# Performance work log

Measured on AMD Instinct MI355X. Metric: run time of the kernel, lower is better.

Reference implementation:

```python
import jax, jax.numpy as jnp
import numpy as np
from jax import lax


def _ramp_filter_real(size):
    # torch ramp_filter: spatial-domain ramp, FFT is purely real (even symmetric)
    image_n = np.concatenate([np.arange(1, size // 2 + 1, 2),
                              np.arange(size // 2 - 1, 0, -2)]).astype(np.float64)
    f = np.zeros(size, dtype=np.float64)
    f[0] = 0.25
    f[1::2] = -1.0 / (np.pi * image_n) ** 2
    return (2.0 * np.real(np.fft.fft(f))).astype(np.float32)  # [size]


def setup_inputs() -> dict:
    key = jax.random.key(0)
    # sinogram: [B, C, detector_bins, n_angles]
    x = jax.random.normal(key, (4, 1, 512, 180), dtype=jnp.float32)
    return {"x": x}


def reference(x):
    B, C, S, A = x.shape  # S = in_size = it_size (circle=True), A = n_angles
    # ---- ramp filtering along detector axis (axis=2) ----
    pad_to = max(64, 1 << int(np.ceil(np.log2(2 * S))))
    xp = jnp.pad(x, ((0, 0), (0, 0), (0, pad_to - S), (0, 0)))
    ramp = jnp.asarray(_ramp_filter_real(pad_to))
    # original multiplies by complex filter r*(1+i); imag part of ifft is 0 for real x,
    # so real part equals standard ramp filtering
    Xf = jnp.fft.fft(xp, axis=2)
    filt = (ramp * (1.0 + 1.0j)).astype(jnp.complex64)
    xfilt = jnp.real(jnp.fft.ifft(Xf * filt[None, None, :, None], axis=2))
    xfilt = xfilt[:, :, :S, :].astype(x.dtype)  # [B,C,S,A]

    # ---- backprojection ----
    unit = jnp.linspace(-1.0, 1.0, S, dtype=x.dtype)
    ygrid, xgrid = jnp.meshgrid(unit, unit, indexing="ij")  # torch.meshgrid 'ij'
    thetas = (jnp.arange(A, dtype=x.dtype) * (np.pi / 180.0)).astype(x.dtype)
    # t coordinate in [-sqrt2, sqrt2]: [A,S,S]
    t = (xgrid[None] * jnp.cos(thetas)[:, None, None]
         - ygrid[None] * jnp.sin(thetas)[:, None, None])
    # grid_sample bilinear, align_corners=True, zeros padding; X coord selects angle i exactly
    p = (t + 1.0) * 0.5 * (S - 1)
    p0 = jnp.floor(p)
    w = (p - p0).astype(x.dtype)
    i0 = p0.astype(jnp.int32)
    i1 = i0 + 1
    v0 = ((i0 >= 0) & (i0 < S)).astype(x.dtype)
    v1 = ((i1 >= 0) & (i1 < S)).astype(x.dtype)
    i0c = jnp.clip(i0, 0, S - 1)
    i1c = jnp.clip(i1, 0, S - 1)

    xa = jnp.moveaxis(xfilt, 3, 0)  # [A,B,C,S]

    def body(acc, inp):
        xa_a, i0a, i1a, wa, v0a, v1a = inp
        g = (xa_a[:, :, i0a] * v0a * (1.0 - wa)
             + xa_a[:, :, i1a] * v1a * wa)  # [B,C,S,S]
        return acc + g, None

    reco0 = jnp.zeros((B, C, S, S), dtype=x.dtype)
    reco, _ = lax.scan(body, reco0, (xa, i0c, i1c, w, v0, v1))

    # circle mask + normalization
    mask = (xgrid ** 2 + ygrid ** 2) <= 1.0
    reco = jnp.where(mask[None, None], reco, 0.0)
    reco = reco * (np.pi / (2.0 * A))
    return reco
```

## Files before the change

### kernel.cpp

```cpp
#include <hip/hip_runtime.h>
#include <math.h>

namespace {

constexpr int BB  = 4;
constexpr int SS  = 512;
constexpr int AA  = 180;
constexpr int PAD = 112;
constexpr int ROWBUF = SS + 2 * PAD;

__global__ __launch_bounds__(256) void ramp_filter_kernel(
    const float* __restrict__ x, float* __restrict__ xf) {
  __shared__ __align__(16) float xs[2][2][256];
  __shared__ __align__(16) float G[2][528];
  const int t  = threadIdx.x;
  const int a0 = blockIdx.x * 2;
  const int b  = blockIdx.y;

  const float s  = (float)(M_PI / 360.0);
  const float cc = (float)(-2.0 / (M_PI * M_PI)) * s;
  for (int i = t; i < 528; i += 256) {
    { int kk = i;     float d = (float)(2 * kk - 511); G[0][i] = (kk < 512) ? cc / (d * d) : 0.0f; }
    { int kk = i + 1; float d = (float)(2 * kk - 511); G[1][i] = (kk < 512) ? cc / (d * d) : 0.0f; }
  }

  const float* xb = x + (size_t)b * (SS * AA) + a0;
  {
    int m = t;
    float2 v = *(const float2*)(xb + (size_t)m * AA);
    xs[0][m & 1][m >> 1] = v.x;  xs[1][m & 1][m >> 1] = v.y;
    m = t + 256;
    float2 v2 = *(const float2*)(xb + (size_t)m * AA);
    xs[0][m & 1][m >> 1] = v2.x; xs[1][m & 1][m >> 1] = v2.y;
  }
  __syncthreads();

  const int col = t >> 7;
  const int p   = (t >> 6) & 1;
  const int idx = t & 63;
  const float* Gp = G[p];
  const float* xv = xs[col][1 - p];

  float acc[4] = {0.f, 0.f, 0.f, 0.f};
  float W[8];
  {
    const int A0 = 4 * idx + 252;
    float4 w0 = *(const float4*)(Gp + A0);
    float4 w1 = *(const float4*)(Gp + A0 + 4);
    W[0] = w0.x; W[1] = w0.y; W[2] = w0.z; W[3] = w0.w;
    W[4] = w1.x; W[5] = w1.y; W[6] = w1.z; W[7] = w1.w;
  }

#pragma unroll
  for (int q = 0; q < 64; ++q) {
    const float4 xq = *(const float4*)(xv + 4 * q);
    float4 nw;
    if (q != 63) nw = *(const float4*)(Gp + (4 * idx + 252 - 4 * (q + 1)));
#pragma unroll
    for (int r = 0; r < 4; ++r) {
      acc[r] = fmaf(W[3 + r], xq.x, acc[r]);
      acc[r] = fmaf(W[2 + r], xq.y, acc[r]);
      acc[r] = fmaf(W[1 + r], xq.z, acc[r]);
      acc[r] = fmaf(W[0 + r], xq.w, acc[r]);
    }
    if (q != 63) {
      W[7] = W[3]; W[6] = W[2]; W[5] = W[1]; W[4] = W[0];
      W[0] = nw.x; W[1] = nw.y; W[2] = nw.z; W[3] = nw.w;
    }
  }

  const float selfc = 0.5f * s;
  const float* xsp = xs[col][p];
  float* orow = xf + ((size_t)(b * AA + a0 + col)) * SS;
#pragma unroll
  for (int r = 0; r < 4; ++r) {
    orow[p + 8 * idx + 2 * r] = fmaf(selfc, xsp[4 * idx + r], acc[r]);
  }
}

__global__ __launch_bounds__(256) void backproject_kernel(
    const float* __restrict__ xf, float* __restrict__ out) {
  __shared__ __align__(16) float rows[2][3][ROWBUF];
  __shared__ float2 trig_s[45];

  const int t     = threadIdx.x;
  const int w     = t >> 6;
  const int lane  = t & 63;
  const int tx    = blockIdx.x;
  const int ty    = blockIdx.y;
  const int b     = blockIdx.z >> 2;
  const int chunk = blockIdx.z & 3;
  const int a0    = chunk * 45;

  for (int i = t; i < 2 * 3 * 2 * PAD; i += 256) {
    int rr = i / (2 * PAD);
    int o  = i - rr * (2 * PAD);
    int off = (o < PAD) ? o : (o + SS);
    rows[rr / 3][rr % 3][off] = 0.0f;
  }
  if (t < 45) {
    float th = (float)(a0 + t) * (float)(M_PI / 180.0);
    float sn, cn;
    sincosf(th, &sn, &cn);
    trig_s[t] = make_float2(cn * 255.5f, sn * 255.5f);
  }

  const float* xf_src = xf + ((size_t)b * AA + a0) * SS;

  auto stage = [&](int g, int buf) {
    const float* base = xf_src + (size_t)(g * 3) * SS;
    {
      const int s = w;
      const float* gp = base + (s >> 1) * SS + (s & 1) * 256 + lane * 4;
      void* lp = (void*)&rows[buf][s >> 1][PAD + (s & 1) * 256];
      __builtin_amdgcn_global_load_lds(
          (const __attribute__((address_space(1))) void*)gp,
          (__attribute__((address_space(3))) void*)lp, 16, 0, 0);
    }
    if (w < 2) {
      const int s = 4 + w;
      const float* gp = base + (s >> 1) * SS + (s & 1) * 256 + lane * 4;
      void* lp = (void*)&rows[buf][s >> 1][PAD + (s & 1) * 256];
      __builtin_amdgcn_global_load_lds(
          (const __attribute__((address_space(1))) void*)gp,
          (__attribute__((address_space(3))) void*)lp, 16, 0, 0);
    }
  };

  const int gx = tx * 64 + lane;
  const float step = 2.0f / 511.0f;
  const float xg = __fadd_rn(-1.0f, __fmul_rn((float)gx, step));
  float dy[8];
#pragma unroll
  for (int kk = 0; kk < 8; ++kk) {
    int gy = ty * 32 + w + 4 * kk;
    dy[kk] = -__fadd_rn(-1.0f, __fmul_rn((float)gy, step));
  }

  const float Kp = 255.5f + (float)PAD;
  float acc[8] = {0.f, 0.f, 0.f, 0.f, 0.f, 0.f, 0.f, 0.f};

  stage(0, 0);
  __syncthreads();

  int buf = 0;
  for (int g = 0; g < 15; ++g) {
    if (g + 1 < 15) stage(g + 1, buf ^ 1);
#pragma unroll
    for (int aa = 0; aa < 3; ++aa) {
      const float2 cs = trig_s[g * 3 + aa];
      const float base = fmaf(xg, cs.x, Kp);
      const float* R = rows[buf][aa];
#pragma unroll
      for (int kk = 0; kk < 8; ++kk) {
        float p  = fmaf(dy[kk], cs.y, base);
        int   i0 = (int)p;
#if __has_builtin(__builtin_amdgcn_fractf)
        float wt = __builtin_amdgcn_fractf(p);
#else
        float wt = p - floorf(p);
#endif
        float v0 = R[i0];
        float v1 = R[i0 + 1];
        acc[kk] = fmaf(wt, v1 - v0, acc[kk] + v0);
      }
    }
    __syncthreads();
    buf ^= 1;
  }

  const float xx = __fmul_rn(xg, xg);
#pragma unroll
  for (int kk = 0; kk < 8; ++kk) {
    float ss = __fadd_rn(xx, __fmul_rn(dy[kk], dy[kk]));
    if (ss <= 1.0f) {
      int gy = ty * 32 + w + 4 * kk;
      unsafeAtomicAdd(&out[((size_t)b * SS + gy) * SS + gx], acc[kk]);
    }
  }
}

}

extern "C" void kernel_launch(void* const* d_in, const int* in_sizes, int n_in,
                              void* d_out, int out_size, void* d_ws, size_t ws_size,
                              hipStream_t stream) {
  const float* x   = (const float*)d_in[0];
  float*       out = (float*)d_out;
  float*       xf  = (float*)d_ws;

  hipMemsetAsync(d_out, 0, (size_t)out_size * sizeof(float), stream);
  ramp_filter_kernel<<<dim3(AA / 2, BB), 256, 0, stream>>>(x, xf);
  backproject_kernel<<<dim3(8, 16, 16), 256, 0, stream>>>(xf, out);
}
```

Before: 106.9 us.

## Fuse zeroing, ramp filter and backprojection into one cooperative kernel

Replaces the memset plus two kernel launches with a single cooperative-grid kernel of 512 blocks. Each block zeroes part of the output, the first 360 blocks run the ramp filter, and after a grid-wide sync every block runs the backprojection. The backprojection is re-tiled so each thread covers two output columns and 90 angles instead of 45, which halves the number of atomic-add passes. Neighbouring taps are read as one paired LDS load. A two-kernel fallback runs if the cooperative launch fails. The grid sync adds its own cost, and fewer, larger blocks may reduce occupancy.

Result: slower. 218.5 us (+104.5%).

```diff
diff --git a/kernel.cpp b/kernel.cpp
--- a/kernel.cpp
+++ b/kernel.cpp
@@ -1,5 +1,8 @@
 #include <hip/hip_runtime.h>
+#include <hip/hip_cooperative_groups.h>
 #include <math.h>
+
+namespace cg = cooperative_groups;
 
 namespace {
 
@@ -9,37 +12,57 @@
 constexpr int PAD = 112;
 constexpr int ROWBUF = SS + 2 * PAD;
 
-__global__ __launch_bounds__(256) void ramp_filter_kernel(
-    const float* __restrict__ x, float* __restrict__ xf) {
-  __shared__ __align__(16) float xs[2][2][256];
-  __shared__ __align__(16) float G[2][528];
-  const int t  = threadIdx.x;
-  const int a0 = blockIdx.x * 2;
-  const int b  = blockIdx.y;
+struct RampShared {
+  float xs[2][2][256];
+  float G[2][528];
+};
+struct BpShared {
+  float  rows[2][3][ROWBUF];
+  float2 trig[90];
+};
+constexpr size_t SMEM_BYTES =
+    sizeof(BpShared) > sizeof(RampShared) ? sizeof(BpShared) : sizeof(RampShared);
+
+__device__ __forceinline__ float2 lds_load_pair(const float* p) {
+  float2 v;
+  __builtin_memcpy(&v, p, sizeof(float2));
+  return v;
+}
+
+__device__ __forceinline__ void phase0_zero(int bid, int t, float* out) {
+  float4 z = make_float4(0.f, 0.f, 0.f, 0.f);
+  ((float4*)out)[bid * 512 + t]       = z;
+  ((float4*)out)[bid * 512 + 256 + t] = z;
+}
+
+__device__ __forceinline__ void phase1_ramp(int bid, int t, const float* x,
+                                            float* xf, RampShared& S) {
+  const int b  = bid / 90;
+  const int a0 = (bid - b * 90) * 2;
 
   const float s  = (float)(M_PI / 360.0);
   const float cc = (float)(-2.0 / (M_PI * M_PI)) * s;
   for (int i = t; i < 528; i += 256) {
-    { int kk = i;     float d = (float)(2 * kk - 511); G[0][i] = (kk < 512) ? cc / (d * d) : 0.0f; }
-    { int kk = i + 1; float d = (float)(2 * kk - 511); G[1][i] = (kk < 512) ? cc / (d * d) : 0.0f; }
+    { int kk = i;     float d = (float)(2 * kk - 511); S.G[0][i] = (kk < 512) ? cc / (d * d) : 0.0f; }
+    { int kk = i + 1; float d = (float)(2 * kk - 511); S.G[1][i] = (kk < 512) ? cc / (d * d) : 0.0f; }
   }
 
   const float* xb = x + (size_t)b * (SS * AA) + a0;
   {
     int m = t;
     float2 v = *(const float2*)(xb + (size_t)m * AA);
-    xs[0][m & 1][m >> 1] = v.x;  xs[1][m & 1][m >> 1] = v.y;
+    S.xs[0][m & 1][m >> 1] = v.x;  S.xs[1][m & 1][m >> 1] = v.y;
     m = t + 256;
     float2 v2 = *(const float2*)(xb + (size_t)m * AA);
-    xs[0][m & 1][m >> 1] = v2.x; xs[1][m & 1][m >> 1] = v2.y;
+    S.xs[0][m & 1][m >> 1] = v2.x; S.xs[1][m & 1][m >> 1] = v2.y;
   }
   __syncthreads();
 
   const int col = t >> 7;
   const int p   = (t >> 6) & 1;
   const int idx = t & 63;
-  const float* Gp = G[p];
-  const float* xv = xs[col][1 - p];
+  const float* Gp = S.G[p];
+  const float* xv = S.xs[col][1 - p];
 
   float acc[4] = {0.f, 0.f, 0.f, 0.f};
   float W[8];
@@ -70,39 +93,34 @@
   }
 
   const float selfc = 0.5f * s;
-  const float* xsp = xs[col][p];
+  const float* xsp = S.xs[col][p];
   float* orow = xf + ((size_t)(b * AA + a0 + col)) * SS;
 #pragma unroll
-  for (int r = 0; r < 4; ++r) {
+  for (int r = 0; r < 4; ++r)
     orow[p + 8 * idx + 2 * r] = fmaf(selfc, xsp[4 * idx + r], acc[r]);
-  }
-}
-
-__global__ __launch_bounds__(256) void backproject_kernel(
-    const float* __restrict__ xf, float* __restrict__ out) {
-  __shared__ __align__(16) float rows[2][3][ROWBUF];
-  __shared__ float2 trig_s[45];
-
-  const int t     = threadIdx.x;
-  const int w     = t >> 6;
-  const int lane  = t & 63;
-  const int tx    = blockIdx.x;
-  const int ty    = blockIdx.y;
-  const int b     = blockIdx.z >> 2;
-  const int chunk = blockIdx.z & 3;
-  const int a0    = chunk * 45;
+}
+
+__device__ __forceinline__ void phase2_bp(int bid, int t, const float* xf,
+                                          float* out, BpShared& S) {
+  const int tx   = bid & 3;
+  const int ty   = (bid >> 2) & 15;
+  const int z    = bid >> 6;
+  const int b    = z >> 1;
+  const int a0   = (z & 1) * 90;
+  const int w    = t >> 6;
+  const int lane = t & 63;
 
   for (int i = t; i < 2 * 3 * 2 * PAD; i += 256) {
     int rr = i / (2 * PAD);
     int o  = i - rr * (2 * PAD);
     int off = (o < PAD) ? o : (o + SS);
-    rows[rr / 3][rr % 3][off] = 0.0f;
-  }
-  if (t < 45) {
+    S.rows[rr / 3][rr % 3][off] = 0.0f;
+  }
+  if (t < 90) {
     float th = (float)(a0 + t) * (float)(M_PI / 180.0);
     float sn, cn;
     sincosf(th, &sn, &cn);
-    trig_s[t] = make_float2(cn * 255.5f, sn * 255.5f);
+    S.trig[t] = make_float2(cn * 255.5f, sn * 255.5f);
   }
 
   const float* xf_src = xf + ((size_t)b * AA + a0) * SS;
@@ -110,26 +128,27 @@
   auto stage = [&](int g, int buf) {
     const float* base = xf_src + (size_t)(g * 3) * SS;
     {
-      const int s = w;
-      const float* gp = base + (s >> 1) * SS + (s & 1) * 256 + lane * 4;
-      void* lp = (void*)&rows[buf][s >> 1][PAD + (s & 1) * 256];
+      const int sg = w;
+      const float* gp = base + (sg >> 1) * SS + (sg & 1) * 256 + lane * 4;
+      void* lp = (void*)&S.rows[buf][sg >> 1][PAD + (sg & 1) * 256];
       __builtin_amdgcn_global_load_lds(
           (const __attribute__((address_space(1))) void*)gp,
           (__attribute__((address_space(3))) void*)lp, 16, 0, 0);
     }
     if (w < 2) {
-      const int s = 4 + w;
-      const float* gp = base + (s >> 1) * SS + (s & 1) * 256 + lane * 4;
-      void* lp = (void*)&rows[buf][s >> 1][PAD + (s & 1) * 256];
+      const int sg = 4 + w;
+      const float* gp = base + (sg >> 1) * SS + (sg & 1) * 256 + lane * 4;
+      void* lp = (void*)&S.rows[buf][sg >> 1][PAD + (sg & 1) * 256];
       __builtin_amdgcn_global_load_lds(
           (const __attribute__((address_space(1))) void*)gp,
           (__attribute__((address_space(3))) void*)lp, 16, 0, 0);
     }
   };
 
-  const int gx = tx * 64 + lane;
+  const int gx0 = tx * 128 + lane;
   const float step = 2.0f / 511.0f;
-  const float xg = __fadd_rn(-1.0f, __fmul_rn((float)gx, step));
+  const float xg0 = __fadd_rn(-1.0f, __fmul_rn((float)gx0, step));
+  const float xg1 = __fadd_rn(-1.0f, __fmul_rn((float)(gx0 + 64), step));
   float dy[8];
 #pragma unroll
   for (int kk = 0; kk < 8; ++kk) {
@@ -138,46 +157,81 @@
   }
 
   const float Kp = 255.5f + (float)PAD;
-  float acc[8] = {0.f, 0.f, 0.f, 0.f, 0.f, 0.f, 0.f, 0.f};
+  float acc0[8], acc1[8];
+#pragma unroll
+  for (int kk = 0; kk < 8; ++kk) { acc0[kk] = 0.f; acc1[kk] = 0.f; }
 
   stage(0, 0);
   __syncthreads();
 
   int buf = 0;
-  for (int g = 0; g < 15; ++g) {
-    if (g + 1 < 15) stage(g + 1, buf ^ 1);
+  for (int g = 0; g < 30; ++g) {
+    if (g + 1 < 30) stage(g + 1, buf ^ 1);
 #pragma unroll
     for (int aa = 0; aa < 3; ++aa) {
-      const float2 cs = trig_s[g * 3 + aa];
-      const float base = fmaf(xg, cs.x, Kp);
-      const float* R = rows[buf][aa];
+      const float2 cs = S.trig[g * 3 + aa];
+      const float base0 = fmaf(xg0, cs.x, Kp);
+      const float base1 = fmaf(xg1, cs.x, Kp);
+      const float* R = S.rows[buf][aa];
 #pragma unroll
       for (int kk = 0; kk < 8; ++kk) {
-        float p  = fmaf(dy[kk], cs.y, base);
-        int   i0 = (int)p;
+        float p0 = fmaf(dy[kk], cs.y, base0);
+        float p1 = fmaf(dy[kk], cs.y, base1);
+        int   i0 = (int)p0;
+        int   i1 = (int)p1;
 #if __has_builtin(__builtin_amdgcn_fractf)
-        float wt = __builtin_amdgcn_fractf(p);
+        float w0 = __builtin_amdgcn_fractf(p0);
+        float w1 = __builtin_amdgcn_fractf(p1);
 #else
-        float wt = p - floorf(p);
+        float w0 = p0 - floorf(p0);
+        float w1 = p1 - floorf(p1);
 #endif
-        float v0 = R[i0];
-        float v1 = R[i0 + 1];
-        acc[kk] = fmaf(wt, v1 - v0, acc[kk] + v0);
+        float2 ab0 = lds_load_pair(R + i0);
+        float2 ab1 = lds_load_pair(R + i1);
+        acc0[kk] = fmaf(w0, ab0.y - ab0.x, acc0[kk] + ab0.x);
+        acc1[kk] = fmaf(w1, ab1.y - ab1.x, acc1[kk] + ab1.x);
       }
     }
     __syncthreads();
     buf ^= 1;
   }
 
-  const float xx = __fmul_rn(xg, xg);
+  const float xx0 = __fmul_rn(xg0, xg0);
+  const float xx1 = __fmul_rn(xg1, xg1);
 #pragma unroll
   for (int kk = 0; kk < 8; ++kk) {
-    float ss = __fadd_rn(xx, __fmul_rn(dy[kk], dy[kk]));
-    if (ss <= 1.0f) {
-      int gy = ty * 32 + w + 4 * kk;
-      unsafeAtomicAdd(&out[((size_t)b * SS + gy) * SS + gx], acc[kk]);
-    }
-  }
+    int gy = ty * 32 + w + 4 * kk;
+    float yy = __fmul_rn(dy[kk], dy[kk]);
+    float s0 = __fadd_rn(xx0, yy);
+    float s1 = __fadd_rn(xx1, yy);
+    float* orow = out + ((size_t)b * SS + gy) * SS;
+    if (s0 <= 1.0f) unsafeAtomicAdd(&orow[gx0], acc0[kk]);
+    if (s1 <= 1.0f) unsafeAtomicAdd(&orow[gx0 + 64], acc1[kk]);
+  }
+}
+
+__global__ __launch_bounds__(256, 4) void fused_coop(
+    const float* __restrict__ x, float* __restrict__ xf, float* __restrict__ out) {
+  __shared__ __align__(16) char smem[SMEM_BYTES];
+  const int t   = threadIdx.x;
+  const int bid = blockIdx.x;
+  phase0_zero(bid, t, out);
+  if (bid < 360) phase1_ramp(bid, t, x, xf, *(RampShared*)smem);
+  cg::this_grid().sync();
+  phase2_bp(bid, t, xf, out, *(BpShared*)smem);
+}
+
+__global__ __launch_bounds__(256, 4) void k_pre(
+    const float* __restrict__ x, float* __restrict__ xf, float* __restrict__ out) {
+  __shared__ __align__(16) char smem[sizeof(RampShared)];
+  const int t = threadIdx.x, bid = blockIdx.x;
+  phase0_zero(bid, t, out);
+  if (bid < 360) phase1_ramp(bid, t, x, xf, *(RampShared*)smem);
+}
+__global__ __launch_bounds__(256, 4) void k_bp(
+    const float* __restrict__ xf, float* __restrict__ out) {
+  __shared__ __align__(16) char smem[sizeof(BpShared)];
+  phase2_bp(blockIdx.x, threadIdx.x, xf, out, *(BpShared*)smem);
 }
 
 }
@@ -189,7 +243,11 @@
   float*       out = (float*)d_out;
   float*       xf  = (float*)d_ws;
 
-  hipMemsetAsync(d_out, 0, (size_t)out_size * sizeof(float), stream);
-  ramp_filter_kernel<<<dim3(AA / 2, BB), 256, 0, stream>>>(x, xf);
-  backproject_kernel<<<dim3(8, 16, 16), 256, 0, stream>>>(xf, out);
-}
+  void* args[3] = {(void*)&x, (void*)&xf, (void*)&out};
+  hipError_t err = hipLaunchCooperativeKernel((const void*)fused_coop,
+                                              dim3(512), dim3(256), args, 0, stream);
+  if (err != hipSuccess) {
+    k_pre<<<dim3(512), 256, 0, stream>>>(x, xf, out);
+    k_bp<<<dim3(512), 256, 0, stream>>>(xf, out);
+  }
+}
```

## Exploit point symmetry in backprojection and fuse output zeroing into ramp kernel

Applied to the files above, without the earlier changes.

Backprojection now computes each pixel together with its point-reflected mirror (511-gx, 511-gy). For the mirror pixel, t becomes -t, which reads the detector row reversed. The kernel stores forward and reversed rows interleaved as float2 in LDS, so one 16-byte LDS read serves both pixels, and the grid is halved in x. Staging switches from global_load_lds to register loads that are written to LDS after compute. The separate memset is removed and the output is zeroed inside the ramp filter kernel, cutting one launch. The cost is more registers and LDS traffic per block, plus relying on exact mirror symmetry of the floating-point grid.

New measurement: 99.86 us. 6.5% less time.

```diff
diff --git a/kernel.cpp b/kernel.cpp
--- a/kernel.cpp
+++ b/kernel.cpp
@@ -7,13 +7,22 @@
 constexpr int SS  = 512;
 constexpr int AA  = 180;
 constexpr int PAD = 112;
-constexpr int ROWBUF = SS + 2 * PAD;
-
-__global__ __launch_bounds__(256) void ramp_filter_kernel(
-    const float* __restrict__ x, float* __restrict__ xf) {
+constexpr int RB  = SS + 2 * PAD;
+
+typedef float v2f __attribute__((ext_vector_type(2)));
+
+__global__ __launch_bounds__(256) void ramp_zero_kernel(
+    const float* __restrict__ x, float* __restrict__ xf, float* __restrict__ out) {
+  const int t = threadIdx.x;
+  {
+    const int bid = blockIdx.y * 90 + blockIdx.x;
+    float4 z = make_float4(0.f, 0.f, 0.f, 0.f);
+    for (int i = bid * 256 + t; i < (BB * SS * SS) / 4; i += 360 * 256)
+      ((float4*)out)[i] = z;
+  }
+
   __shared__ __align__(16) float xs[2][2][256];
   __shared__ __align__(16) float G[2][528];
-  const int t  = threadIdx.x;
   const int a0 = blockIdx.x * 2;
   const int b  = blockIdx.y;
 
@@ -73,15 +82,14 @@
   const float* xsp = xs[col][p];
   float* orow = xf + ((size_t)(b * AA + a0 + col)) * SS;
 #pragma unroll
-  for (int r = 0; r < 4; ++r) {
+  for (int r = 0; r < 4; ++r)
     orow[p + 8 * idx + 2 * r] = fmaf(selfc, xsp[4 * idx + r], acc[r]);
-  }
-}
-
-__global__ __launch_bounds__(256) void backproject_kernel(
+}
+
+__global__ __launch_bounds__(256, 4) void backproject_kernel(
     const float* __restrict__ xf, float* __restrict__ out) {
-  __shared__ __align__(16) float rows[2][3][ROWBUF];
-  __shared__ float2 trig_s[45];
+  __shared__ __align__(16) v2f P[2][3][RB];
+  __shared__ float2 trig[45];
 
   const int t     = threadIdx.x;
   const int w     = t >> 6;
@@ -93,37 +101,37 @@
   const int a0    = chunk * 45;
 
   for (int i = t; i < 2 * 3 * 2 * PAD; i += 256) {
-    int rr = i / (2 * PAD);
-    int o  = i - rr * (2 * PAD);
-    int off = (o < PAD) ? o : (o + SS);
-    rows[rr / 3][rr % 3][off] = 0.0f;
+    int bu  = i / 672;
+    int rem = i - bu * 672;
+    int rr  = rem / 224;
+    int o   = rem - rr * 224;
+    int j   = (o < PAD) ? o : (o + SS);
+    P[bu][rr][j] = (v2f){0.f, 0.f};
   }
   if (t < 45) {
     float th = (float)(a0 + t) * (float)(M_PI / 180.0);
     float sn, cn;
     sincosf(th, &sn, &cn);
-    trig_s[t] = make_float2(cn * 255.5f, sn * 255.5f);
-  }
-
-  const float* xf_src = xf + ((size_t)b * AA + a0) * SS;
-
-  auto stage = [&](int g, int buf) {
-    const float* base = xf_src + (size_t)(g * 3) * SS;
-    {
-      const int s = w;
-      const float* gp = base + (s >> 1) * SS + (s & 1) * 256 + lane * 4;
-      void* lp = (void*)&rows[buf][s >> 1][PAD + (s & 1) * 256];
-      __builtin_amdgcn_global_load_lds(
-          (const __attribute__((address_space(1))) void*)gp,
-          (__attribute__((address_space(3))) void*)lp, 16, 0, 0);
-    }
-    if (w < 2) {
-      const int s = 4 + w;
-      const float* gp = base + (s >> 1) * SS + (s & 1) * 256 + lane * 4;
-      void* lp = (void*)&rows[buf][s >> 1][PAD + (s & 1) * 256];
-      __builtin_amdgcn_global_load_lds(
-          (const __attribute__((address_space(1))) void*)gp,
-          (__attribute__((address_space(3))) void*)lp, 16, 0, 0);
+    trig[t] = make_float2(cn * 255.5f, sn * 255.5f);
+  }
+
+  const float* src = xf + ((size_t)b * AA + a0) * SS;
+
+  float2 fw[3], rv[3];
+  auto ld = [&](int g) {
+    const float* base = src + (size_t)(g * 3) * SS;
+#pragma unroll
+    for (int k = 0; k < 3; ++k) {
+      const float* row = base + k * SS;
+      fw[k] = *(const float2*)(row + 2 * t);
+      rv[k] = *(const float2*)(row + 510 - 2 * t);
+    }
+  };
+  auto st = [&](int buf) {
+#pragma unroll
+    for (int k = 0; k < 3; ++k) {
+      float4 q = make_float4(fw[k].x, rv[k].y, fw[k].y, rv[k].x);
+      *(float4*)&P[buf][k][PAD + 2 * t] = q;
     }
   };
 
@@ -138,45 +146,61 @@
   }
 
   const float Kp = 255.5f + (float)PAD;
-  float acc[8] = {0.f, 0.f, 0.f, 0.f, 0.f, 0.f, 0.f, 0.f};
-
-  stage(0, 0);
+  v2f acc[8];
+#pragma unroll
+  for (int kk = 0; kk < 8; ++kk) acc[kk] = (v2f){0.f, 0.f};
+
+  ld(0);
+  st(0);
   __syncthreads();
 
   int buf = 0;
   for (int g = 0; g < 15; ++g) {
-    if (g + 1 < 15) stage(g + 1, buf ^ 1);
+    if (g + 1 < 15) ld(g + 1);
 #pragma unroll
     for (int aa = 0; aa < 3; ++aa) {
-      const float2 cs = trig_s[g * 3 + aa];
+      const float2 cs = trig[g * 3 + aa];
       const float base = fmaf(xg, cs.x, Kp);
-      const float* R = rows[buf][aa];
+      const v2f* R = P[buf][aa];
 #pragma unroll
       for (int kk = 0; kk < 8; ++kk) {
-        float p  = fmaf(dy[kk], cs.y, base);
-        int   i0 = (int)p;
+        float p = fmaf(dy[kk], cs.y, base);
+        int   I = (int)p;
 #if __has_builtin(__builtin_amdgcn_fractf)
-        float wt = __builtin_amdgcn_fractf(p);
+        float wq = __builtin_amdgcn_fractf(p);
 #else
-        float wt = p - floorf(p);
+        float wq = p - floorf(p);
 #endif
-        float v0 = R[i0];
-        float v1 = R[i0 + 1];
-        acc[kk] = fmaf(wt, v1 - v0, acc[kk] + v0);
+        struct { v2f a, b; } q;
+        __builtin_memcpy(&q, R + I, 16);
+        v2f d  = q.b - q.a;
+        v2f wv = {wq, wq};
+        acc[kk] = (acc[kk] + q.a) + wv * d;
       }
     }
-    __syncthreads();
-    buf ^= 1;
-  }
-
-  const float xx = __fmul_rn(xg, xg);
+    if (g + 1 < 15) {
+      st(buf ^ 1);
+      __syncthreads();
+      buf ^= 1;
+    }
+  }
+
+  const int gxm  = 511 - gx;
+  const float xgm = __fadd_rn(-1.0f, __fmul_rn((float)gxm, step));
+  const float xx  = __fmul_rn(xg, xg);
+  const float xxm = __fmul_rn(xgm, xgm);
 #pragma unroll
   for (int kk = 0; kk < 8; ++kk) {
-    float ss = __fadd_rn(xx, __fmul_rn(dy[kk], dy[kk]));
-    if (ss <= 1.0f) {
-      int gy = ty * 32 + w + 4 * kk;
-      unsafeAtomicAdd(&out[((size_t)b * SS + gy) * SS + gx], acc[kk]);
-    }
+    int gy  = ty * 32 + w + 4 * kk;
+    float yg = -dy[kk];
+    float s0 = __fadd_rn(xx, __fmul_rn(yg, yg));
+    if (s0 <= 1.0f)
+      unsafeAtomicAdd(&out[((size_t)b * SS + gy) * SS + gx], acc[kk].x);
+    int gym = 511 - gy;
+    float ygm = __fadd_rn(-1.0f, __fmul_rn((float)gym, step));
+    float s1 = __fadd_rn(xxm, __fmul_rn(ygm, ygm));
+    if (s1 <= 1.0f)
+      unsafeAtomicAdd(&out[((size_t)b * SS + gym) * SS + gxm], acc[kk].y);
   }
 }
 
@@ -189,7 +213,6 @@
   float*       out = (float*)d_out;
   float*       xf  = (float*)d_ws;
 
-  hipMemsetAsync(d_out, 0, (size_t)out_size * sizeof(float), stream);
-  ramp_filter_kernel<<<dim3(AA / 2, BB), 256, 0, stream>>>(x, xf);
-  backproject_kernel<<<dim3(8, 16, 16), 256, 0, stream>>>(xf, out);
-}
+  ramp_zero_kernel<<<dim3(AA / 2, BB), 256, 0, stream>>>(x, xf, out);
+  backproject_kernel<<<dim3(4, 16, 16), 256, 0, stream>>>(xf, out);
+}
```
